# Kernel tuning notes

Hardware: AMD Instinct MI355X
Metric: run time of the kernel (lower is better)

Reference implementation:

```python
import jax, jax.numpy as jnp
import numpy as np

NEG_SLOPE = 0.01  # LeakyReLU default
STRIDE = 5        # group_length // 4
EPS = 1e-5        # RMSNorm eps


def leaky_relu(x):
    return jnp.where(x >= 0, x, NEG_SLOPE * x)


def rmsnorm(x, w):
    return x * jax.lax.rsqrt(jnp.mean(x * x, axis=-1, keepdims=True) + EPS) * w


def s6(x, fc1_w, fc1_b, fc2_w, fc2_b, fc3_w, fc3_b, A):
    # x: [B, L, D] with D = 2*d_model; A: [D, N]
    delta = jax.nn.softplus(x @ fc1_w.T + fc1_b)        # [B, L, D]
    Bm = x @ fc2_w.T + fc2_b                             # [B, L, N]
    Cm = x @ fc3_w.T + fc3_b                             # [B, L, N]
    dA = jnp.exp(jnp.einsum('bld,dn->bldn', delta, A))   # [B, L, D, N]
    dBx = jnp.einsum('bld,bln,bld->bldn', delta, Bm, x)  # delta * B * x

    def step(h, inp):
        dA_t, dBx_t = inp
        h = dA_t * h + dBx_t
        return h, h

    B_, L, D, N = dA.shape
    h0 = jnp.zeros((B_, D, N), dtype=x.dtype)
    _, hs = jax.lax.scan(step, h0, (jnp.swapaxes(dA, 0, 1), jnp.swapaxes(dBx, 0, 1)))
    hs = jnp.swapaxes(hs, 0, 1)                          # [B, L, D, N]
    return jnp.einsum('bln,bldn->bld', Cm, hs)           # [B, L, D]


def setup_inputs() -> dict:
    key = jax.random.key(0)
    ks = iter(jax.random.split(key, 32))

    def rn(shape, scale=0.02):
        return scale * jax.random.normal(next(ks), shape, dtype=jnp.float32)

    B, band, gl, d, N, L = 256, 189, 20, 128, 128, 34
    di = 2 * d
    return {
        'x': jax.random.normal(next(ks), (B, 1, band), dtype=jnp.float32),
        'conv_w': rn((d, 1, gl)), 'conv_b': rn((d,)),
        'norm_w': jnp.ones((d,), jnp.float32),
        'inp_w': rn((di, d)), 'inp_b': rn((di,)),
        'seqconv_w': rn((L, L, 3)), 'seqconv_b': rn((L,)),
        'convlin_w': rn((di, di)), 'convlin_b': rn((di,)),
        'fc1_w': rn((di, di)), 'fc1_b': rn((di,)),
        'fc2_w': rn((N, di)), 'fc2_b': rn((N,)),
        'fc3_w': rn((N, di)), 'fc3_b': rn((N,)),
        'A': jnp.ones((di, N), jnp.float32) / jnp.sqrt(jnp.float32(N)),
        'D_w': rn((di, d)), 'D_b': rn((di,)),
        'out_w': rn((d, di)), 'out_b': rn((d,)),
        'fnn1_w': rn((64, L * d)), 'fnn1_b': rn((64,)),
        'fnn2_w': rn((32, 64)), 'fnn2_b': rn((32,)),
    }


def reference(x, conv_w, conv_b, norm_w, inp_w, inp_b, seqconv_w, seqconv_b,
              convlin_w, convlin_b, fc1_w, fc1_b, fc2_w, fc2_b, fc3_w, fc3_b,
              A, D_w, D_b, out_w, out_b, fnn1_w, fnn1_b, fnn2_w, fnn2_b):
    # group division: Conv1d(1, d, k=20, stride=5) + LeakyReLU
    g = jax.lax.conv_general_dilated(x, conv_w, (STRIDE,), [(0, 0)],
                                     dimension_numbers=('NCH', 'OIH', 'NCH'))
    g = leaky_relu(g + conv_b[None, :, None])            # [B, d, L]
    h = jnp.swapaxes(g, 1, 2)                            # [B, L, d]
    # Mamba block
    xn = rmsnorm(h, norm_w)
    xp = xn @ inp_w.T + inp_b                            # [B, L, 2d]
    # Conv1d(seq_len, seq_len, k=3, pad=1): seq axis L is the channel dim
    xc = jax.lax.conv_general_dilated(xp, seqconv_w, (1,), [(1, 1)],
                                      dimension_numbers=('NCH', 'OIH', 'NCH'))
    xc = jax.nn.silu(xc + seqconv_b[None, :, None])
    xc = xc @ convlin_w.T + convlin_b                    # [B, L, 2d]
    xs = s6(xc, fc1_w, fc1_b, fc2_w, fc2_b, fc3_w, fc3_b, A)
    y = jax.nn.silu(xs) * jax.nn.silu(xn @ D_w.T + D_b)  # gated
    y = y @ out_w.T + out_b                              # [B, L, d]
    # FNN head
    f = y.reshape(y.shape[0], -1)                        # [B, L*d]
    f = leaky_relu(f @ fnn1_w.T + fnn1_b)
    return f @ fnn2_w.T + fnn2_b                         # [B, 32]
```

## Files before the change

kernel.cpp:

```cpp
#include <hip/hip_runtime.h>
#include <math.h>


#define NB    256
#define LL    34
#define DD    128
#define DI    256
#define NN    128
#define MM    (NB*LL)

using u16 = unsigned short;
typedef __attribute__((ext_vector_type(8))) short short8;
typedef __attribute__((ext_vector_type(4))) float f32x4;

__device__ __forceinline__ float silu_f(float x)  { return x / (1.f + __expf(-x)); }
__device__ __forceinline__ float softplus_f(float x) {
    return fmaxf(x, 0.f) + __logf(1.f + __expf(-fabsf(x)));
}
__device__ __forceinline__ float leaky_f(float x) { return (x >= 0.f) ? x : 0.01f * x; }

__device__ __forceinline__ u16 f2bf(float x) {
    unsigned u = __float_as_uint(x);
    return (u16)((u + 0x7FFF + ((u >> 16) & 1)) >> 16);
}
__device__ __forceinline__ float bf2f(u16 h) {
    return __uint_as_float(((unsigned)h) << 16);
}
__device__ __forceinline__ void f2pair(float v, u16* h, u16* l) {
    u16 hh = f2bf(v);
    *h = hh;
    *l = f2bf(v - bf2f(hh));
}

__global__ __launch_bounds__(256)
void prep_all_k(const float* __restrict__ inp_w, const float* __restrict__ D_w,
                const float* __restrict__ fc1_w, const float* __restrict__ fc2_w,
                const float* __restrict__ fc3_w, const float* __restrict__ convlin_w,
                const float* __restrict__ out_w,
                const float* __restrict__ inp_b, const float* __restrict__ D_b,
                const float* __restrict__ fc1_b, const float* __restrict__ fc2_b,
                const float* __restrict__ fc3_b,
                const float* __restrict__ W1, const float* __restrict__ A,
                u16* __restrict__ wc1h, u16* __restrict__ wc1l,
                u16* __restrict__ wc3h, u16* __restrict__ wc3l,
                u16* __restrict__ cvh,  u16* __restrict__ cvl,
                u16* __restrict__ owh,  u16* __restrict__ owl,
                float* __restrict__ bias1, float* __restrict__ bias3,
                float* __restrict__ W1T, int* __restrict__ flag)
{
    const int bx  = blockIdx.x;
    const int tid = threadIdx.x;
    __shared__ float tile[64][65];

    if (bx < 1152) {
        int i = bx * 256 + tid;
        if (i < 65536) {
            float v = (i < 32768) ? inp_w[i] : D_w[i - 32768];
            f2pair(v, &wc1h[i], &wc1l[i]);
        } else if (i < 196608) {
            int j = i - 65536;
            float v = (j < 65536) ? fc1_w[j] : (j < 98304 ? fc2_w[j - 65536] : fc3_w[j - 98304]);
            f2pair(v, &wc3h[j], &wc3l[j]);
        } else if (i < 262144) {
            int j = i - 196608;
            f2pair(convlin_w[j], &cvh[j], &cvl[j]);
        } else if (i < 294912) {
            int j = i - 262144;
            f2pair(out_w[j], &owh[j], &owl[j]);
        }
        if (i < 512)  bias1[i] = (i < 256) ? inp_b[i] : D_b[i - 256];
        else if (i < 1024) {
            int j = i - 512;
            bias3[j] = (j < 256) ? fc1_b[j] : (j < 384 ? fc2_b[j - 256] : fc3_b[j - 384]);
        }
    } else if (bx < 1220) {
        const int bt = bx - 1152;
        for (int p = 0; p < 16; p++) {
            int idx = tid + p * 256;
            int r = idx >> 6, c = idx & 63;
            tile[r][c] = W1[(size_t)r * 4352 + bt * 64 + c];
        }
        __syncthreads();
        for (int p = 0; p < 16; p++) {
            int idx = tid + p * 256;
            int cc = idx >> 6, rr = idx & 63;
            W1T[(size_t)(bt * 64 + cc) * 64 + rr] = tile[rr][cc];
        }
    } else {
        __shared__ int s;
        if (tid == 0) s = 1;
        __syncthreads();
        bool ok = true;
        for (int k = 0; k < 128; k++) {
            int idx = tid + k * 256;
            ok &= (A[idx] == A[idx & ~127]);
        }
        if (!ok) s = 0;
        __syncthreads();
        if (tid == 0) *flag = s;
    }
}

__global__ __launch_bounds__(128)
void conv_norm_k(const float* __restrict__ x, const float* __restrict__ cw,
                 const float* __restrict__ cb, const float* __restrict__ nw,
                 u16* __restrict__ XNh, u16* __restrict__ XNl)
{
    int bl = blockIdx.x;
    int b = bl / LL, l = bl % LL;
    int c = threadIdx.x;
    const float* xr = x + (size_t)b * 189 + l * 5;
    float g = cb[c];
    #pragma unroll
    for (int k = 0; k < 20; k++) g = fmaf(xr[k], cw[c * 20 + k], g);
    g = leaky_f(g);

    float s = g * g;
    #pragma unroll
    for (int m = 32; m >= 1; m >>= 1) s += __shfl_xor(s, m);
    __shared__ float wsum[2];
    if ((threadIdx.x & 63) == 0) wsum[threadIdx.x >> 6] = s;
    __syncthreads();
    float mean = (wsum[0] + wsum[1]) * (1.f / 128.f);
    float inv = 1.f / sqrtf(mean + 1e-5f);
    float v = g * inv * nw[c];
    f2pair(v, &XNh[(size_t)bl * DD + c], &XNl[(size_t)bl * DD + c]);
}

template <int K, int EPI>
__global__ __launch_bounds__(256)
void mgemm_k(const u16* __restrict__ Ah, const u16* __restrict__ Al,
             const u16* __restrict__ Wh, const u16* __restrict__ Wl,
             const float* __restrict__ bias,
             float* __restrict__ Y, int ldy,
             u16* __restrict__ Yh, u16* __restrict__ Yl,
             u16* __restrict__ BC)
{
    const int tid  = threadIdx.x;
    const int r0   = blockIdx.x * 128;
    const int c0   = blockIdx.y * 64;
    const int wave = tid >> 6;
    const int lane = tid & 63;
    const int wm   = wave & 1;
    const int wn   = wave >> 1;
    const int l15  = lane & 15;
    const int lq   = lane >> 4;

    __shared__ u16 sAh[128][40];
    __shared__ u16 sAl[128][40];
    __shared__ u16 sBh[64][40];
    __shared__ u16 sBl[64][40];

    f32x4 acc[4][2];
    #pragma unroll
    for (int i = 0; i < 4; i++)
        #pragma unroll
        for (int j = 0; j < 2; j++) acc[i][j] = (f32x4){0.f, 0.f, 0.f, 0.f};

    const int a_row = tid >> 1;
    const int a_kb  = (tid & 1) * 16;
    const int b_row = tid >> 2;
    const int b_ko  = (tid & 3) * 8;

    for (int k0 = 0; k0 < K; k0 += 32) {
        const u16* ga = Ah + (size_t)(r0 + a_row) * K + k0 + a_kb;
        const u16* gl = Al + (size_t)(r0 + a_row) * K + k0 + a_kb;
        short8 vh0 = *(const short8*)(ga);
        short8 vh1 = *(const short8*)(ga + 8);
        short8 vl0 = *(const short8*)(gl);
        short8 vl1 = *(const short8*)(gl + 8);
        const u16* gb = Wh + (size_t)(c0 + b_row) * K + k0 + b_ko;
        const u16* gc = Wl + (size_t)(c0 + b_row) * K + k0 + b_ko;
        short8 wb = *(const short8*)(gb);
        short8 wc = *(const short8*)(gc);

        *(short8*)&sAh[a_row][a_kb]     = vh0;
        *(short8*)&sAh[a_row][a_kb + 8] = vh1;
        *(short8*)&sAl[a_row][a_kb]     = vl0;
        *(short8*)&sAl[a_row][a_kb + 8] = vl1;
        *(short8*)&sBh[b_row][b_ko] = wb;
        *(short8*)&sBl[b_row][b_ko] = wc;
        __syncthreads();

        short8 fah[4], fal[4], fbh[2], fbl[2];
        #pragma unroll
        for (int i = 0; i < 4; i++) {
            fah[i] = *(const short8*)&sAh[wm * 64 + i * 16 + l15][lq * 8];
            fal[i] = *(const short8*)&sAl[wm * 64 + i * 16 + l15][lq * 8];
        }
        #pragma unroll
        for (int j = 0; j < 2; j++) {
            fbh[j] = *(const short8*)&sBh[wn * 32 + j * 16 + l15][lq * 8];
            fbl[j] = *(const short8*)&sBl[wn * 32 + j * 16 + l15][lq * 8];
        }
        #pragma unroll
        for (int i = 0; i < 4; i++)
            #pragma unroll
            for (int j = 0; j < 2; j++) {
                acc[i][j] = __builtin_amdgcn_mfma_f32_16x16x32_bf16(fah[i], fbh[j], acc[i][j], 0, 0, 0);
                acc[i][j] = __builtin_amdgcn_mfma_f32_16x16x32_bf16(fah[i], fbl[j], acc[i][j], 0, 0, 0);
                acc[i][j] = __builtin_amdgcn_mfma_f32_16x16x32_bf16(fal[i], fbh[j], acc[i][j], 0, 0, 0);
            }
        __syncthreads();
    }

    #pragma unroll
    for (int i = 0; i < 4; i++) {
        int gr = r0 + wm * 64 + i * 16 + lq * 4;
        #pragma unroll
        for (int j = 0; j < 2; j++) {
            int gc = c0 + wn * 32 + j * 16 + l15;
            float bb = bias[gc];
            #pragma unroll
            for (int r = 0; r < 4; r++) {
                float v = acc[i][j][r] + bb;
                if (EPI == 1 || EPI == 3) { if (gc < 256) v = softplus_f(v); }
                if (EPI == 2) {
                    u16 hh, ll;
                    f2pair(v, &hh, &ll);
                    Yh[(size_t)(gr + r) * ldy + gc] = hh;
                    Yl[(size_t)(gr + r) * ldy + gc] = ll;
                } else {
                    Y[(size_t)(gr + r) * ldy + gc] = v;
                    if (EPI == 3 && gc >= 256) {
                        u16 hh, ll;
                        f2pair(v, &hh, &ll);
                        u16* rb = BC + (size_t)(gr + r) * 1024
                                     + ((gc < 384) ? 0 : 256) + (gc & 127);
                        rb[0]   = hh;
                        rb[128] = ll;
                    }
                }
            }
        }
    }
}

__global__ __launch_bounds__(256)
void seqconv_k(const float* __restrict__ XP, int ldxp,
               const float* __restrict__ w, const float* __restrict__ bias,
               u16* __restrict__ XCh, u16* __restrict__ XCl)
{
    const int b   = blockIdx.x;
    const int tid = threadIdx.x;
    const int tx  = tid & 63;
    const int ty  = tid >> 6;
    const int j0  = tx * 4;

    __shared__ float sx[LL][264];
    __shared__ float sw[LL][112];

    for (int idx = tid; idx < LL * 256; idx += 256) {
        int li = idx >> 8, jj = idx & 255;
        sx[li][jj + 1] = XP[(size_t)(b * LL + li) * ldxp + jj];
    }
    if (tid < LL) { sx[tid][0] = 0.f; sx[tid][257] = 0.f; }
    for (int idx = tid; idx < LL * LL * 3; idx += 256) {
        int lo = idx / 102;
        int rem = idx - lo * 102;
        int li = rem / 3;
        int k  = rem - li * 3;
        sw[li][lo * 3 + k] = w[idx];
    }
    __syncthreads();

    const int base = ty * 9 - (ty == 3 ? 1 : 0);
    const int cnt  = (ty < 2) ? 9 : 8;

    float acc[9][4];
    #pragma unroll
    for (int i = 0; i < 9; i++)
        #pragma unroll
        for (int jj = 0; jj < 4; jj++) acc[i][jj] = 0.f;

    for (int li = 0; li < LL; li++) {
        float4 xa = *(const float4*)&sx[li][j0];
        float2 xb = *(const float2*)&sx[li][j0 + 4];
        float xv[6] = {xa.x, xa.y, xa.z, xa.w, xb.x, xb.y};
        const float* swr = &sw[li][0];
        #pragma unroll
        for (int i = 0; i < 9; i++) {
            if (i < cnt) {
                int lo3 = (base + i) * 3;
                float w0 = swr[lo3 + 0];
                float w1 = swr[lo3 + 1];
                float w2 = swr[lo3 + 2];
                #pragma unroll
                for (int jj = 0; jj < 4; jj++) {
                    acc[i][jj] = fmaf(w0, xv[jj],     acc[i][jj]);
                    acc[i][jj] = fmaf(w1, xv[jj + 1], acc[i][jj]);
                    acc[i][jj] = fmaf(w2, xv[jj + 2], acc[i][jj]);
                }
            }
        }
    }

    #pragma unroll
    for (int i = 0; i < 9; i++) {
        if (i < cnt) {
            int lo = base + i;
            float bb = bias[lo];
            ushort4 oh, ol;
            float v0 = silu_f(acc[i][0] + bb);
            float v1 = silu_f(acc[i][1] + bb);
            float v2 = silu_f(acc[i][2] + bb);
            float v3 = silu_f(acc[i][3] + bb);
            f2pair(v0, &oh.x, &ol.x);
            f2pair(v1, &oh.y, &ol.y);
            f2pair(v2, &oh.z, &ol.z);
            f2pair(v3, &oh.w, &ol.w);
            size_t o = (size_t)(b * LL + lo) * DI + j0;
            *(ushort4*)&XCh[o] = oh;
            *(ushort4*)&XCl[o] = ol;
        }
    }
}

__global__ __launch_bounds__(256)
void ssd_scan_k(const int* __restrict__ flag,
                const float* __restrict__ dBC,
                const u16* __restrict__ BC,
                const u16* __restrict__ Xh, const u16* __restrict__ Xl,
                const float* __restrict__ A,
                const float* __restrict__ DG,
                u16* __restrict__ Gh, u16* __restrict__ Gl)
{
    if (*flag == 0) return;
    const int b    = blockIdx.x;
    const int tid  = threadIdx.x;
    const int wave = tid >> 6;
    const int lane = tid & 63;
    const int l15  = lane & 15;
    const int lq   = lane >> 4;

    __shared__ u16 sBh[48][136], sBl[48][136];
    __shared__ u16 sCh[48][136], sCl[48][136];
    __shared__ float sM[48][49];

    const u16* base = BC + (size_t)b * LL * 1024;
    for (int idx = tid; idx < LL * 16; idx += 256) {
        int l = idx >> 4, c = (idx & 15) << 3;
        const u16* row = base + l * 1024;
        *(short8*)&sBh[l][c] = *(const short8*)&row[c];
        *(short8*)&sBl[l][c] = *(const short8*)&row[128 + c];
        *(short8*)&sCh[l][c] = *(const short8*)&row[256 + c];
        *(short8*)&sCl[l][c] = *(const short8*)&row[384 + c];
    }
    __syncthreads();

    for (int tt = wave; tt < 9; tt += 4) {
        int ti = tt / 3, tj = tt - ti * 3;
        f32x4 acc = (f32x4){0.f, 0.f, 0.f, 0.f};
        #pragma unroll
        for (int ks = 0; ks < 4; ks++) {
            short8 ch = *(const short8*)&sCh[ti * 16 + l15][ks * 32 + lq * 8];
            short8 cl = *(const short8*)&sCl[ti * 16 + l15][ks * 32 + lq * 8];
            short8 bh = *(const short8*)&sBh[tj * 16 + l15][ks * 32 + lq * 8];
            short8 bl = *(const short8*)&sBl[tj * 16 + l15][ks * 32 + lq * 8];
            acc = __builtin_amdgcn_mfma_f32_16x16x32_bf16(ch, bh, acc, 0, 0, 0);
            acc = __builtin_amdgcn_mfma_f32_16x16x32_bf16(ch, bl, acc, 0, 0, 0);
            acc = __builtin_amdgcn_mfma_f32_16x16x32_bf16(cl, bh, acc, 0, 0, 0);
        }
        #pragma unroll
        for (int r = 0; r < 4; r++)
            sM[ti * 16 + lq * 4 + r][tj * 16 + l15] = acc[r];
    }
    __syncthreads();

    const int d = tid;
    const float a_d = A[(size_t)d * NN];
    const float* pDel = dBC + (size_t)b * LL * 512 + d;
    const u16* pXh = Xh + (size_t)b * LL * 256 + d;
    const u16* pXl = Xl + (size_t)b * LL * 256 + d;

    float u[LL], eS[LL];
    float S = 0.f;
    #pragma unroll
    for (int l = 0; l < LL; l++) {
        float dl = pDel[l * 512];
        S = fmaf(dl, a_d, S);
        eS[l] = __expf(S);
        float xv = bf2f(pXh[l * 256]) + bf2f(pXl[l * 256]);
        u[l] = __expf(-S) * dl * xv;
    }

    const float* pG = DG + (size_t)b * LL * 512 + 256 + d;
    u16* pGh = Gh + (size_t)b * LL * 256 + d;
    u16* pGl = Gl + (size_t)b * LL * 256 + d;
    #pragma unroll
    for (int l = 0; l < LL; l++) {
        float acc = 0.f;
        for (int t = 0; t <= l; t++) acc = fmaf(sM[l][t], u[t], acc);
        float xs = eS[l] * acc;
        float g = silu_f(xs) * silu_f(pG[l * 512]);
        u16 hh, ll2;
        f2pair(g, &hh, &ll2);
        pGh[l * 256] = hh;
        pGl[l * 256] = ll2;
    }
}

__global__ __launch_bounds__(256)
void scan_fb_k(const int* __restrict__ flag,
               const float* __restrict__ dBC,
               const u16*  __restrict__ Xh, const u16* __restrict__ Xl,
               const float* __restrict__ A,
               const float* __restrict__ DG,
               u16* __restrict__ Gh, u16* __restrict__ Gl)
{
    if (*flag != 0) return;
    const int b  = blockIdx.y;
    const int d0 = blockIdx.x * 64;
    const int tid = threadIdx.x;
    const int sub = tid & 15;
    const int pg  = tid >> 4;
    const int dbase = d0 + pg * 4;
    const int nA = sub * 4;

    float a[4][8], h[4][8];
    #pragma unroll
    for (int dd = 0; dd < 4; dd++) {
        const float* Ar = A + (size_t)(dbase + dd) * NN;
        float4 q0 = *(const float4*)(Ar + nA);
        float4 q1 = *(const float4*)(Ar + 64 + nA);
        a[dd][0]=q0.x; a[dd][1]=q0.y; a[dd][2]=q0.z; a[dd][3]=q0.w;
        a[dd][4]=q1.x; a[dd][5]=q1.y; a[dd][6]=q1.z; a[dd][7]=q1.w;
        #pragma unroll
        for (int j = 0; j < 8; j++) h[dd][j] = 0.f;
    }

    const float* pD  = dBC + (size_t)b * LL * 512 + dbase;
    const float* pBC = dBC + (size_t)b * LL * 512 + 256 + nA;
    const u16*  pXh = Xh  + (size_t)b * LL * 256 + dbase;
    const u16*  pXl = Xl  + (size_t)b * LL * 256 + dbase;
    const float* pG  = DG  + (size_t)b * LL * 512 + 256 + dbase;
    u16* pGh = Gh + (size_t)b * LL * 256 + dbase;
    u16* pGl = Gl + (size_t)b * LL * 256 + dbase;

    for (int l = 0; l < LL; l++) {
        float4  cD  = *(const float4*)(pD);
        ushort4 cXh = *(const ushort4*)(pXh);
        ushort4 cXl = *(const ushort4*)(pXl);
        float4 cB0 = *(const float4*)(pBC);
        float4 cB1 = *(const float4*)(pBC + 64);
        float4 cC0 = *(const float4*)(pBC + 128);
        float4 cC1 = *(const float4*)(pBC + 192);
        pD += 512; pBC += 512; pXh += 256; pXl += 256;

        float xv[4] = { bf2f(cXh.x) + bf2f(cXl.x), bf2f(cXh.y) + bf2f(cXl.y),
                        bf2f(cXh.z) + bf2f(cXl.z), bf2f(cXh.w) + bf2f(cXl.w) };
        float dl[4] = {cD.x, cD.y, cD.z, cD.w};
        float dx[4] = {cD.x * xv[0], cD.y * xv[1], cD.z * xv[2], cD.w * xv[3]};
        float bv[8] = {cB0.x,cB0.y,cB0.z,cB0.w,cB1.x,cB1.y,cB1.z,cB1.w};
        float cv[8] = {cC0.x,cC0.y,cC0.z,cC0.w,cC1.x,cC1.y,cC1.z,cC1.w};

        float accd[4] = {0.f, 0.f, 0.f, 0.f};
        #pragma unroll
        for (int dd = 0; dd < 4; dd++)
            #pragma unroll
            for (int j = 0; j < 8; j++) {
                float dA = __expf(dl[dd] * a[dd][j]);
                h[dd][j] = fmaf(dA, h[dd][j], dx[dd] * bv[j]);
                accd[dd] = fmaf(cv[j], h[dd][j], accd[dd]);
            }
        #pragma unroll
        for (int dd = 0; dd < 4; dd++) {
            float v = accd[dd];
            v += __shfl_xor(v, 1);
            v += __shfl_xor(v, 2);
            v += __shfl_xor(v, 4);
            v += __shfl_xor(v, 8);
            accd[dd] = v;
        }
        if (sub == 0) {
            float4 dg = *(const float4*)(pG);
            ushort4 oh, ol;
            float g0 = silu_f(accd[0]) * silu_f(dg.x);
            float g1 = silu_f(accd[1]) * silu_f(dg.y);
            float g2 = silu_f(accd[2]) * silu_f(dg.z);
            float g3 = silu_f(accd[3]) * silu_f(dg.w);
            f2pair(g0, &oh.x, &ol.x);
            f2pair(g1, &oh.y, &ol.y);
            f2pair(g2, &oh.z, &ol.z);
            f2pair(g3, &oh.w, &ol.w);
            *(ushort4*)pGh = oh;
            *(ushort4*)pGl = ol;
        }
        pG += 512; pGh += 256; pGl += 256;
    }
}

__global__ __launch_bounds__(256)
void fnn1_k(const float* __restrict__ F, const float* __restrict__ W1T,
            float* __restrict__ partials)
{
    const int btile = blockIdx.x;
    const int kc    = blockIdx.y;
    const int tid   = threadIdx.x;
    __shared__ float sf[16][260];
    for (int i = tid; i < 16 * 256; i += 256) {
        int r = i >> 8, c = i & 255;
        sf[r][c] = F[(size_t)(btile * 16 + r) * 4352 + kc * 256 + c];
    }
    __syncthreads();

    const int o  = tid & 63;
    const int bq = tid >> 6;
    const float* w = W1T + (size_t)(kc * 256) * 64 + o;
    float acc[4] = {0.f, 0.f, 0.f, 0.f};
    for (int k = 0; k < 256; k += 4) {
        float w0 = w[(size_t)(k + 0) * 64];
        float w1 = w[(size_t)(k + 1) * 64];
        float w2 = w[(size_t)(k + 2) * 64];
        float w3 = w[(size_t)(k + 3) * 64];
        #pragma unroll
        for (int bj = 0; bj < 4; bj++) {
            float4 f4 = *(const float4*)&sf[bq * 4 + bj][k];
            acc[bj] = fmaf(w0, f4.x, acc[bj]);
            acc[bj] = fmaf(w1, f4.y, acc[bj]);
            acc[bj] = fmaf(w2, f4.z, acc[bj]);
            acc[bj] = fmaf(w3, f4.w, acc[bj]);
        }
    }
    #pragma unroll
    for (int bj = 0; bj < 4; bj++)
        partials[(size_t)kc * 16384 + (btile * 16 + bq * 4 + bj) * 64 + o] = acc[bj];
}

__global__ __launch_bounds__(64)
void fnn2_k(const float* __restrict__ partials,
            const float* __restrict__ B1,
            const float* __restrict__ W2, const float* __restrict__ B2,
            float* __restrict__ out)
{
    int b = blockIdx.x;
    int t = threadIdx.x;
    __shared__ float s1[64];
    float acc = B1[t];
    #pragma unroll
    for (int kc = 0; kc < 17; kc++)
        acc += partials[(size_t)kc * 16384 + b * 64 + t];
    s1[t] = leaky_f(acc);
    __syncthreads();

    if (t < 32) {
        float acc2 = B2[t];
        const float* w2 = W2 + t * 64;
        #pragma unroll
        for (int j = 0; j < 64; j++) acc2 = fmaf(s1[j], w2[j], acc2);
        out[(size_t)b * 32 + t] = acc2;
    }
}

extern "C" void kernel_launch(void* const* d_in, const int* in_sizes, int n_in,
                              void* d_out, int out_size, void* d_ws, size_t ws_size,
                              hipStream_t stream)
{
    const float* x        = (const float*)d_in[0];
    const float* conv_w   = (const float*)d_in[1];
    const float* conv_b   = (const float*)d_in[2];
    const float* norm_w   = (const float*)d_in[3];
    const float* inp_w    = (const float*)d_in[4];
    const float* inp_b    = (const float*)d_in[5];
    const float* seqconv_w= (const float*)d_in[6];
    const float* seqconv_b= (const float*)d_in[7];
    const float* convlin_w= (const float*)d_in[8];
    const float* convlin_b= (const float*)d_in[9];
    const float* fc1_w    = (const float*)d_in[10];
    const float* fc1_b    = (const float*)d_in[11];
    const float* fc2_w    = (const float*)d_in[12];
    const float* fc2_b    = (const float*)d_in[13];
    const float* fc3_w    = (const float*)d_in[14];
    const float* fc3_b    = (const float*)d_in[15];
    const float* A        = (const float*)d_in[16];
    const float* D_w      = (const float*)d_in[17];
    const float* D_b      = (const float*)d_in[18];
    const float* out_w    = (const float*)d_in[19];
    const float* out_b    = (const float*)d_in[20];
    const float* fnn1_w   = (const float*)d_in[21];
    const float* fnn1_b   = (const float*)d_in[22];
    const float* fnn2_w   = (const float*)d_in[23];
    const float* fnn2_b   = (const float*)d_in[24];

    char* W = (char*)d_ws;
    float* buf1  = (float*)(W + 0);
    float* buf3  = (float*)(W + 17825792);
    u16*   xnh   = (u16*)  (W + 35651584);
    u16*   xnl   = (u16*)  (W + 37879808);
    u16*   xc2h  = (u16*)  (W + 35651584);
    float* fout  = (float*)(W + 35651584);
    u16*   xc2l  = (u16*)  (W + 40108032);
    u16*   xch   = (u16*)  (W + 44564480);
    u16*   xcl   = (u16*)  (W + 49020928);
    float* w1t   = (float*)(W + 53477376);
    u16*   wc1h  = (u16*)  (W + 54591488);
    u16*   wc1l  = (u16*)  (W + 54722560);
    u16*   wc3h  = (u16*)  (W + 54853632);
    u16*   wc3l  = (u16*)  (W + 55115776);
    u16*   cvh   = (u16*)  (W + 55377920);
    u16*   cvl   = (u16*)  (W + 55508992);
    u16*   owh   = (u16*)  (W + 55640064);
    u16*   owl   = (u16*)  (W + 55705600);
    float* bias1 = (float*)(W + 55771136);
    float* bias3 = (float*)(W + 55773184);
    int*   uflag = (int*)  (W + 55775232);
    u16* gateh = xch;
    u16* gatel = xcl;
    u16* bcpair = (u16*)buf1;
    float* partials = buf3;

    prep_all_k<<<1221, 256, 0, stream>>>(inp_w, D_w, fc1_w, fc2_w, fc3_w,
                                         convlin_w, out_w,
                                         inp_b, D_b, fc1_b, fc2_b, fc3_b,
                                         fnn1_w, A,
                                         wc1h, wc1l, wc3h, wc3l, cvh, cvl,
                                         owh, owl, bias1, bias3, w1t, uflag);

    conv_norm_k<<<MM, 128, 0, stream>>>(x, conv_w, conv_b, norm_w, xnh, xnl);

    mgemm_k<128, 0><<<dim3(MM / 128, 8), 256, 0, stream>>>(
        xnh, xnl, wc1h, wc1l, bias1, buf1, 512, nullptr, nullptr, nullptr);

    seqconv_k<<<NB, 256, 0, stream>>>(buf1, 512, seqconv_w, seqconv_b, xch, xcl);

    mgemm_k<256, 2><<<dim3(MM / 128, 4), 256, 0, stream>>>(
        xch, xcl, cvh, cvl, convlin_b, nullptr, 256, xc2h, xc2l, nullptr);

    mgemm_k<256, 3><<<dim3(MM / 128, 8), 256, 0, stream>>>(
        xc2h, xc2l, wc3h, wc3l, bias3, buf3, 512, nullptr, nullptr, bcpair);

    ssd_scan_k<<<NB, 256, 0, stream>>>(uflag, buf3, bcpair, xc2h, xc2l, A,
                                       buf1, gateh, gatel);
    scan_fb_k<<<dim3(4, NB), 256, 0, stream>>>(uflag, buf3, xc2h, xc2l, A,
                                               buf1, gateh, gatel);

    mgemm_k<256, 0><<<dim3(MM / 128, 2), 256, 0, stream>>>(
        gateh, gatel, owh, owl, out_b, fout, 128, nullptr, nullptr, nullptr);

    fnn1_k<<<dim3(16, 17), 256, 0, stream>>>(fout, w1t, partials);
    fnn2_k<<<NB, 64, 0, stream>>>(partials, fnn1_b, fnn2_w, fnn2_b,
                                  (float*)d_out);
}
```

Baseline: 220.6 us.

## Fuse SSD scan, out-projection and FNN head into one per-batch kernel

```diff
diff --git a/kernel.cpp b/kernel.cpp
--- a/kernel.cpp
+++ b/kernel.cpp
@@ -33,27 +33,51 @@
 }
 
 __global__ __launch_bounds__(256)
-void prep_all_k(const float* __restrict__ inp_w, const float* __restrict__ D_w,
-                const float* __restrict__ fc1_w, const float* __restrict__ fc2_w,
-                const float* __restrict__ fc3_w, const float* __restrict__ convlin_w,
-                const float* __restrict__ out_w,
-                const float* __restrict__ inp_b, const float* __restrict__ D_b,
-                const float* __restrict__ fc1_b, const float* __restrict__ fc2_b,
-                const float* __restrict__ fc3_b,
-                const float* __restrict__ W1, const float* __restrict__ A,
-                u16* __restrict__ wc1h, u16* __restrict__ wc1l,
-                u16* __restrict__ wc3h, u16* __restrict__ wc3l,
-                u16* __restrict__ cvh,  u16* __restrict__ cvl,
-                u16* __restrict__ owh,  u16* __restrict__ owl,
-                float* __restrict__ bias1, float* __restrict__ bias3,
-                float* __restrict__ W1T, int* __restrict__ flag)
+void prep_conv_k(const float* __restrict__ x, const float* __restrict__ cw,
+                 const float* __restrict__ cb, const float* __restrict__ nw,
+                 u16* __restrict__ XNh, u16* __restrict__ XNl,
+                 const float* __restrict__ inp_w, const float* __restrict__ D_w,
+                 const float* __restrict__ fc1_w, const float* __restrict__ fc2_w,
+                 const float* __restrict__ fc3_w, const float* __restrict__ convlin_w,
+                 const float* __restrict__ out_w,
+                 const float* __restrict__ inp_b, const float* __restrict__ D_b,
+                 const float* __restrict__ fc1_b, const float* __restrict__ fc2_b,
+                 const float* __restrict__ fc3_b,
+                 const float* __restrict__ W1, const float* __restrict__ A,
+                 u16* __restrict__ wc1h, u16* __restrict__ wc1l,
+                 u16* __restrict__ wc3h, u16* __restrict__ wc3l,
+                 u16* __restrict__ cvh,  u16* __restrict__ cvl,
+                 u16* __restrict__ owh,  u16* __restrict__ owl,
+                 float* __restrict__ bias1, float* __restrict__ bias3,
+                 float* __restrict__ W1T, int* __restrict__ flag)
 {
     const int bx  = blockIdx.x;
     const int tid = threadIdx.x;
     __shared__ float tile[64][65];
-
-    if (bx < 1152) {
-        int i = bx * 256 + tid;
+    __shared__ float wsum[4];
+
+    if (bx < 4352) {
+        const int row = tid >> 7;
+        const int c   = tid & 127;
+        const int bl  = bx * 2 + row;
+        const int b   = bl / LL, l = bl % LL;
+        const float* xr = x + (size_t)b * 189 + l * 5;
+        float g = cb[c];
+        #pragma unroll
+        for (int k = 0; k < 20; k++) g = fmaf(xr[k], cw[c * 20 + k], g);
+        g = leaky_f(g);
+
+        float s = g * g;
+        #pragma unroll
+        for (int m = 32; m >= 1; m >>= 1) s += __shfl_xor(s, m);
+        if ((tid & 63) == 0) wsum[tid >> 6] = s;
+        __syncthreads();
+        float mean = (wsum[row * 2] + wsum[row * 2 + 1]) * (1.f / 128.f);
+        float inv = 1.f / sqrtf(mean + 1e-5f);
+        float v = g * inv * nw[c];
+        f2pair(v, &XNh[(size_t)bl * DD + c], &XNl[(size_t)bl * DD + c]);
+    } else if (bx < 5504) {
+        int i = (bx - 4352) * 256 + tid;
         if (i < 65536) {
             float v = (i < 32768) ? inp_w[i] : D_w[i - 32768];
             f2pair(v, &wc1h[i], &wc1l[i]);
@@ -73,8 +97,8 @@
             int j = i - 512;
             bias3[j] = (j < 256) ? fc1_b[j] : (j < 384 ? fc2_b[j - 256] : fc3_b[j - 384]);
         }
-    } else if (bx < 1220) {
-        const int bt = bx - 1152;
+    } else if (bx < 5572) {
+        const int bt = bx - 5504;
         for (int p = 0; p < 16; p++) {
             int idx = tid + p * 256;
             int r = idx >> 6, c = idx & 63;
@@ -99,32 +123,6 @@
         __syncthreads();
         if (tid == 0) *flag = s;
     }
-}
-
-__global__ __launch_bounds__(128)
-void conv_norm_k(const float* __restrict__ x, const float* __restrict__ cw,
-                 const float* __restrict__ cb, const float* __restrict__ nw,
-                 u16* __restrict__ XNh, u16* __restrict__ XNl)
-{
-    int bl = blockIdx.x;
-    int b = bl / LL, l = bl % LL;
-    int c = threadIdx.x;
-    const float* xr = x + (size_t)b * 189 + l * 5;
-    float g = cb[c];
-    #pragma unroll
-    for (int k = 0; k < 20; k++) g = fmaf(xr[k], cw[c * 20 + k], g);
-    g = leaky_f(g);
-
-    float s = g * g;
-    #pragma unroll
-    for (int m = 32; m >= 1; m >>= 1) s += __shfl_xor(s, m);
-    __shared__ float wsum[2];
-    if ((threadIdx.x & 63) == 0) wsum[threadIdx.x >> 6] = s;
-    __syncthreads();
-    float mean = (wsum[0] + wsum[1]) * (1.f / 128.f);
-    float inv = 1.f / sqrtf(mean + 1e-5f);
-    float v = g * inv * nw[c];
-    f2pair(v, &XNh[(size_t)bl * DD + c], &XNl[(size_t)bl * DD + c]);
 }
 
 template <int K, int EPI>
@@ -317,90 +315,6 @@
 }
 
 __global__ __launch_bounds__(256)
-void ssd_scan_k(const int* __restrict__ flag,
-                const float* __restrict__ dBC,
-                const u16* __restrict__ BC,
-                const u16* __restrict__ Xh, const u16* __restrict__ Xl,
-                const float* __restrict__ A,
-                const float* __restrict__ DG,
-                u16* __restrict__ Gh, u16* __restrict__ Gl)
-{
-    if (*flag == 0) return;
-    const int b    = blockIdx.x;
-    const int tid  = threadIdx.x;
-    const int wave = tid >> 6;
-    const int lane = tid & 63;
-    const int l15  = lane & 15;
-    const int lq   = lane >> 4;
-
-    __shared__ u16 sBh[48][136], sBl[48][136];
-    __shared__ u16 sCh[48][136], sCl[48][136];
-    __shared__ float sM[48][49];
-
-    const u16* base = BC + (size_t)b * LL * 1024;
-    for (int idx = tid; idx < LL * 16; idx += 256) {
-        int l = idx >> 4, c = (idx & 15) << 3;
-        const u16* row = base + l * 1024;
-        *(short8*)&sBh[l][c] = *(const short8*)&row[c];
-        *(short8*)&sBl[l][c] = *(const short8*)&row[128 + c];
-        *(short8*)&sCh[l][c] = *(const short8*)&row[256 + c];
-        *(short8*)&sCl[l][c] = *(const short8*)&row[384 + c];
-    }
-    __syncthreads();
-
-    for (int tt = wave; tt < 9; tt += 4) {
-        int ti = tt / 3, tj = tt - ti * 3;
-        f32x4 acc = (f32x4){0.f, 0.f, 0.f, 0.f};
-        #pragma unroll
-        for (int ks = 0; ks < 4; ks++) {
-            short8 ch = *(const short8*)&sCh[ti * 16 + l15][ks * 32 + lq * 8];
-            short8 cl = *(const short8*)&sCl[ti * 16 + l15][ks * 32 + lq * 8];
-            short8 bh = *(const short8*)&sBh[tj * 16 + l15][ks * 32 + lq * 8];
-            short8 bl = *(const short8*)&sBl[tj * 16 + l15][ks * 32 + lq * 8];
-            acc = __builtin_amdgcn_mfma_f32_16x16x32_bf16(ch, bh, acc, 0, 0, 0);
-            acc = __builtin_amdgcn_mfma_f32_16x16x32_bf16(ch, bl, acc, 0, 0, 0);
-            acc = __builtin_amdgcn_mfma_f32_16x16x32_bf16(cl, bh, acc, 0, 0, 0);
-        }
-        #pragma unroll
-        for (int r = 0; r < 4; r++)
-            sM[ti * 16 + lq * 4 + r][tj * 16 + l15] = acc[r];
-    }
-    __syncthreads();
-
-    const int d = tid;
-    const float a_d = A[(size_t)d * NN];
-    const float* pDel = dBC + (size_t)b * LL * 512 + d;
-    const u16* pXh = Xh + (size_t)b * LL * 256 + d;
-    const u16* pXl = Xl + (size_t)b * LL * 256 + d;
-
-    float u[LL], eS[LL];
-    float S = 0.f;
-    #pragma unroll
-    for (int l = 0; l < LL; l++) {
-        float dl = pDel[l * 512];
-        S = fmaf(dl, a_d, S);
-        eS[l] = __expf(S);
-        float xv = bf2f(pXh[l * 256]) + bf2f(pXl[l * 256]);
-        u[l] = __expf(-S) * dl * xv;
-    }
-
-    const float* pG = DG + (size_t)b * LL * 512 + 256 + d;
-    u16* pGh = Gh + (size_t)b * LL * 256 + d;
-    u16* pGl = Gl + (size_t)b * LL * 256 + d;
-    #pragma unroll
-    for (int l = 0; l < LL; l++) {
-        float acc = 0.f;
-        for (int t = 0; t <= l; t++) acc = fmaf(sM[l][t], u[t], acc);
-        float xs = eS[l] * acc;
-        float g = silu_f(xs) * silu_f(pG[l * 512]);
-        u16 hh, ll2;
-        f2pair(g, &hh, &ll2);
-        pGh[l * 256] = hh;
-        pGl[l * 256] = ll2;
-    }
-}
-
-__global__ __launch_bounds__(256)
 void scan_fb_k(const int* __restrict__ flag,
                const float* __restrict__ dBC,
                const u16*  __restrict__ Xh, const u16* __restrict__ Xl,
@@ -490,65 +404,191 @@
     }
 }
 
-__global__ __launch_bounds__(256)
-void fnn1_k(const float* __restrict__ F, const float* __restrict__ W1T,
-            float* __restrict__ partials)
+__global__ __launch_bounds__(512)
+void ssd_tail_k(const int* __restrict__ flag,
+                const float* __restrict__ dBC,
+                const u16* __restrict__ BCp,
+                const u16* __restrict__ Xh, const u16* __restrict__ Xl,
+                const float* __restrict__ A,
+                const float* __restrict__ DG,
+                const u16* __restrict__ gFh, const u16* __restrict__ gFl,
+                const u16* __restrict__ owh, const u16* __restrict__ owl,
+                const float* __restrict__ outb,
+                const float* __restrict__ W1T, const float* __restrict__ B1,
+                const float* __restrict__ W2, const float* __restrict__ B2,
+                float* __restrict__ out)
 {
-    const int btile = blockIdx.x;
-    const int kc    = blockIdx.y;
-    const int tid   = threadIdx.x;
-    __shared__ float sf[16][260];
-    for (int i = tid; i < 16 * 256; i += 256) {
-        int r = i >> 8, c = i & 255;
-        sf[r][c] = F[(size_t)(btile * 16 + r) * 4352 + kc * 256 + c];
+    const int b    = blockIdx.x;
+    const int tid  = threadIdx.x;
+    const int wave = tid >> 6;
+    const int lane = tid & 63;
+    const int l15  = lane & 15;
+    const int lq   = lane >> 4;
+
+    __shared__ __align__(16) char smem[71936];
+    u16  (*sBh)[136] = (u16 (*)[136])(smem);
+    u16  (*sBl)[136] = (u16 (*)[136])(smem + 13056);
+    u16  (*sCh)[136] = (u16 (*)[136])(smem + 26112);
+    u16  (*sCl)[136] = (u16 (*)[136])(smem + 39168);
+    float (*sM)[49]  = (float (*)[49])(smem + 52224);
+    u16  (*sGh)[264] = (u16 (*)[264])(smem);
+    u16  (*sGl)[264] = (u16 (*)[264])(smem + 25344);
+    float* sF        = (float*)(smem + 52224);
+    float* s1p       = (float*)(smem + 69632);
+    float* s1        = (float*)(smem + 71680);
+
+    const bool uni = (*flag != 0);
+    if (uni) {
+        const u16* base = BCp + (size_t)b * LL * 1024;
+        for (int idx = tid; idx < LL * 16; idx += 512) {
+            int l = idx >> 4, c = (idx & 15) << 3;
+            const u16* row = base + l * 1024;
+            *(short8*)&sBh[l][c] = *(const short8*)&row[c];
+            *(short8*)&sBl[l][c] = *(const short8*)&row[128 + c];
+            *(short8*)&sCh[l][c] = *(const short8*)&row[256 + c];
+            *(short8*)&sCl[l][c] = *(const short8*)&row[384 + c];
+        }
+        __syncthreads();
+
+        for (int tt = wave; tt < 9; tt += 8) {
+            int ti = tt / 3, tj = tt - ti * 3;
+            f32x4 acc = (f32x4){0.f, 0.f, 0.f, 0.f};
+            #pragma unroll
+            for (int ks = 0; ks < 4; ks++) {
+                short8 ch = *(const short8*)&sCh[ti * 16 + l15][ks * 32 + lq * 8];
+                short8 cl = *(const short8*)&sCl[ti * 16 + l15][ks * 32 + lq * 8];
+                short8 bh = *(const short8*)&sBh[tj * 16 + l15][ks * 32 + lq * 8];
+                short8 bl = *(const short8*)&sBl[tj * 16 + l15][ks * 32 + lq * 8];
+                acc = __builtin_amdgcn_mfma_f32_16x16x32_bf16(ch, bh, acc, 0, 0, 0);
+                acc = __builtin_amdgcn_mfma_f32_16x16x32_bf16(ch, bl, acc, 0, 0, 0);
+                acc = __builtin_amdgcn_mfma_f32_16x16x32_bf16(cl, bh, acc, 0, 0, 0);
+            }
+            #pragma unroll
+            for (int r = 0; r < 4; r++)
+                sM[ti * 16 + lq * 4 + r][tj * 16 + l15] = acc[r];
+        }
+        __syncthreads();
+
+        if (tid < 256) {
+            const int d = tid;
+            const float a_d = A[(size_t)d * NN];
+            const float* pDel = dBC + (size_t)b * LL * 512 + d;
+            const u16* pXh = Xh + (size_t)b * LL * 256 + d;
+            const u16* pXl = Xl + (size_t)b * LL * 256 + d;
+
+            float u[LL], eS[LL];
+            float S = 0.f;
+            #pragma unroll
+            for (int l = 0; l < LL; l++) {
+                float dl = pDel[l * 512];
+                S = fmaf(dl, a_d, S);
+                eS[l] = __expf(S);
+                float xv = bf2f(pXh[l * 256]) + bf2f(pXl[l * 256]);
+                u[l] = __expf(-S) * dl * xv;
+            }
+
+            const float* pG = DG + (size_t)b * LL * 512 + 256 + d;
+            #pragma unroll
+            for (int l = 0; l < LL; l++) {
+                float acc = 0.f;
+                for (int t = 0; t <= l; t++) acc = fmaf(sM[l][t], u[t], acc);
+                float xs = eS[l] * acc;
+                float g = silu_f(xs) * silu_f(pG[l * 512]);
+                u16 hh, ll2;
+                f2pair(g, &hh, &ll2);
+                sGh[l][d] = hh;
+                sGl[l][d] = ll2;
+            }
+        } else {
+            u16* zh = &sGh[34][0];
+            u16* zl = &sGl[34][0];
+            for (int idx = tid - 256; idx < 14 * 264; idx += 256) {
+                zh[idx] = 0;
+                zl[idx] = 0;
+            }
+        }
+        __syncthreads();
+    } else {
+        for (int idx = tid; idx < LL * 32; idx += 512) {
+            int l = idx >> 5, c = (idx & 31) << 3;
+            *(short8*)&sGh[l][c] = *(const short8*)&gFh[((size_t)b * LL + l) * 256 + c];
+            *(short8*)&sGl[l][c] = *(const short8*)&gFl[((size_t)b * LL + l) * 256 + c];
+        }
+        u16* zh = &sGh[34][0];
+        u16* zl = &sGl[34][0];
+        for (int idx = tid; idx < 14 * 264; idx += 512) {
+            zh[idx] = 0;
+            zl[idx] = 0;
+        }
+        __syncthreads();
+    }
+
+    {
+        const int j0 = wave;
+        f32x4 acc[3];
+        #pragma unroll
+        for (int i = 0; i < 3; i++) acc[i] = (f32x4){0.f, 0.f, 0.f, 0.f};
+        #pragma unroll
+        for (int ks = 0; ks < 8; ks++) {
+            const size_t wo = (size_t)(j0 * 16 + l15) * 256 + ks * 32 + lq * 8;
+            short8 bh = *(const short8*)&owh[wo];
+            short8 bl = *(const short8*)&owl[wo];
+            #pragma unroll
+            for (int i = 0; i < 3; i++) {
+                short8 ah = *(const short8*)&sGh[i * 16 + l15][ks * 32 + lq * 8];
+                short8 al = *(const short8*)&sGl[i * 16 + l15][ks * 32 + lq * 8];
+                acc[i] = __builtin_amdgcn_mfma_f32_16x16x32_bf16(ah, bh, acc[i], 0, 0, 0);
+                acc[i] = __builtin_amdgcn_mfma_f32_16x16x32_bf16(ah, bl, acc[i], 0, 0, 0);
+                acc[i] = __builtin_amdgcn_mfma_f32_16x16x32_bf16(al, bh, acc[i], 0, 0, 0);
+            }
+        }
+        __syncthreads();
+        #pragma unroll
+        for (int i = 0; i < 3; i++) {
+            int row = i * 16 + lq * 4;
+            int col = j0 * 16 + l15;
+            float bb = outb[col];
+            #pragma unroll
+            for (int r = 0; r < 4; r++)
+                if (row + r < LL) sF[(row + r) * 128 + col] = acc[i][r] + bb;
+        }
     }
     __syncthreads();
 
-    const int o  = tid & 63;
-    const int bq = tid >> 6;
-    const float* w = W1T + (size_t)(kc * 256) * 64 + o;
-    float acc[4] = {0.f, 0.f, 0.f, 0.f};
-    for (int k = 0; k < 256; k += 4) {
-        float w0 = w[(size_t)(k + 0) * 64];
-        float w1 = w[(size_t)(k + 1) * 64];
-        float w2 = w[(size_t)(k + 2) * 64];
-        float w3 = w[(size_t)(k + 3) * 64];
-        #pragma unroll
-        for (int bj = 0; bj < 4; bj++) {
-            float4 f4 = *(const float4*)&sf[bq * 4 + bj][k];
-            acc[bj] = fmaf(w0, f4.x, acc[bj]);
-            acc[bj] = fmaf(w1, f4.y, acc[bj]);
-            acc[bj] = fmaf(w2, f4.z, acc[bj]);
-            acc[bj] = fmaf(w3, f4.w, acc[bj]);
-        }
-    }
-    #pragma unroll
-    for (int bj = 0; bj < 4; bj++)
-        partials[(size_t)kc * 16384 + (btile * 16 + bq * 4 + bj) * 64 + o] = acc[bj];
-}
-
-__global__ __launch_bounds__(64)
-void fnn2_k(const float* __restrict__ partials,
-            const float* __restrict__ B1,
-            const float* __restrict__ W2, const float* __restrict__ B2,
-            float* __restrict__ out)
-{
-    int b = blockIdx.x;
-    int t = threadIdx.x;
-    __shared__ float s1[64];
-    float acc = B1[t];
-    #pragma unroll
-    for (int kc = 0; kc < 17; kc++)
-        acc += partials[(size_t)kc * 16384 + b * 64 + t];
-    s1[t] = leaky_f(acc);
+    {
+        const int o = tid & 63;
+        const int q = tid >> 6;
+        const float* wp = W1T + ((size_t)q * 544) * 64 + o;
+        const float* fp = sF + q * 544;
+        float accf = 0.f;
+        for (int k = 0; k < 544; k += 4) {
+            float w0 = wp[(size_t)(k + 0) * 64];
+            float w1 = wp[(size_t)(k + 1) * 64];
+            float w2 = wp[(size_t)(k + 2) * 64];
+            float w3 = wp[(size_t)(k + 3) * 64];
+            accf = fmaf(w0, fp[k + 0], accf);
+            accf = fmaf(w1, fp[k + 1], accf);
+            accf = fmaf(w2, fp[k + 2], accf);
+            accf = fmaf(w3, fp[k + 3], accf);
+        }
+        s1p[q * 64 + o] = accf;
+    }
     __syncthreads();
 
-    if (t < 32) {
-        float acc2 = B2[t];
-        const float* w2 = W2 + t * 64;
-        #pragma unroll
-        for (int j = 0; j < 64; j++) acc2 = fmaf(s1[j], w2[j], acc2);
-        out[(size_t)b * 32 + t] = acc2;
+    if (tid < 64) {
+        float a0 = B1[tid];
+        #pragma unroll
+        for (int q = 0; q < 8; q++) a0 += s1p[q * 64 + tid];
+        s1[tid] = leaky_f(a0);
+    }
+    __syncthreads();
+
+    if (tid < 32) {
+        float a2 = B2[tid];
+        const float* w2 = W2 + tid * 64;
+        #pragma unroll
+        for (int j = 0; j < 64; j++) a2 = fmaf(s1[j], w2[j], a2);
+        out[(size_t)b * 32 + tid] = a2;
     }
 }
 
@@ -588,7 +628,6 @@
     u16*   xnh   = (u16*)  (W + 35651584);
     u16*   xnl   = (u16*)  (W + 37879808);
     u16*   xc2h  = (u16*)  (W + 35651584);
-    float* fout  = (float*)(W + 35651584);
     u16*   xc2l  = (u16*)  (W + 40108032);
     u16*   xch   = (u16*)  (W + 44564480);
     u16*   xcl   = (u16*)  (W + 49020928);
@@ -607,16 +646,14 @@
     u16* gateh = xch;
     u16* gatel = xcl;
     u16* bcpair = (u16*)buf1;
-    float* partials = buf3;
-
-    prep_all_k<<<1221, 256, 0, stream>>>(inp_w, D_w, fc1_w, fc2_w, fc3_w,
-                                         convlin_w, out_w,
-                                         inp_b, D_b, fc1_b, fc2_b, fc3_b,
-                                         fnn1_w, A,
-                                         wc1h, wc1l, wc3h, wc3l, cvh, cvl,
-                                         owh, owl, bias1, bias3, w1t, uflag);
-
-    conv_norm_k<<<MM, 128, 0, stream>>>(x, conv_w, conv_b, norm_w, xnh, xnl);
+
+    prep_conv_k<<<5573, 256, 0, stream>>>(x, conv_w, conv_b, norm_w, xnh, xnl,
+                                          inp_w, D_w, fc1_w, fc2_w, fc3_w,
+                                          convlin_w, out_w,
+                                          inp_b, D_b, fc1_b, fc2_b, fc3_b,
+                                          fnn1_w, A,
+                                          wc1h, wc1l, wc3h, wc3l, cvh, cvl,
+                                          owh, owl, bias1, bias3, w1t, uflag);
 
     mgemm_k<128, 0><<<dim3(MM / 128, 8), 256, 0, stream>>>(
         xnh, xnl, wc1h, wc1l, bias1, buf1, 512, nullptr, nullptr, nullptr);
@@ -629,15 +666,11 @@
     mgemm_k<256, 3><<<dim3(MM / 128, 8), 256, 0, stream>>>(
         xc2h, xc2l, wc3h, wc3l, bias3, buf3, 512, nullptr, nullptr, bcpair);
 
-    ssd_scan_k<<<NB, 256, 0, stream>>>(uflag, buf3, bcpair, xc2h, xc2l, A,
-                                       buf1, gateh, gatel);
     scan_fb_k<<<dim3(4, NB), 256, 0, stream>>>(uflag, buf3, xc2h, xc2l, A,
                                                buf1, gateh, gatel);
 
-    mgemm_k<256, 0><<<dim3(MM / 128, 2), 256, 0, stream>>>(
-        gateh, gatel, owh, owl, out_b, fout, 128, nullptr, nullptr, nullptr);
-
-    fnn1_k<<<dim3(16, 17), 256, 0, stream>>>(fout, w1t, partials);
-    fnn2_k<<<NB, 64, 0, stream>>>(partials, fnn1_b, fnn2_w, fnn2_b,
-                                  (float*)d_out);
-}
+    ssd_tail_k<<<NB, 512, 0, stream>>>(uflag, buf3, bcpair, xc2h, xc2l, A,
+                                       buf1, gateh, gatel, owh, owl, out_b,
+                                       w1t, fnn1_b, fnn2_w, fnn2_b,
+                                       (float*)d_out);
+}
```

Result: faster. 210.9 us (-4.4%).
